# Optimization experiments

Measured on AMD Instinct MI355X. Metric: run time of the kernel, lower is better.

The kernel has to match this reference:

```python
import jax, jax.numpy as jnp
import numpy as np

G = 4096              # number of graphs in batch
NPG = 198             # nodes per graph (fixed by view(-1, 198*2))
N = G * NPG           # total nodes = 811008
DEG = 8               # avg degree
E = N * DEG           # total edges = 6488064
CONV_DIMS = [(2, 20), (20, 15), (15, 10), (10, 5), (5, 2)]
MLP_DIMS = [(396, 200), (200, 100), (100, 50), (50, 10), (10, 2)]


def setup_inputs() -> dict:
    key = jax.random.key(0)
    ks = jax.random.split(key, 64)
    x = jax.random.normal(ks[0], (N, 2), dtype=jnp.float32)
    # block-diagonal edges: endpoints within each 198-node graph, then offset
    src = jax.random.randint(ks[1], (G, E // G), 0, NPG)
    dst = jax.random.randint(ks[2], (G, E // G), 0, NPG)
    off = (jnp.arange(G, dtype=jnp.int32) * NPG)[:, None]
    edge_index = jnp.stack([(src + off).reshape(-1), (dst + off).reshape(-1)]).astype(jnp.int32)
    edge_weight = jax.random.uniform(ks[3], (E,), dtype=jnp.float32)
    inp = {"x": x, "edge_index": edge_index, "edge_weight": edge_weight}
    ki = 4
    for i, (ci, co) in enumerate(CONV_DIMS):
        s = 1.0 / np.sqrt(ci)
        inp[f"w_rel{i}"] = jax.random.normal(ks[ki], (co, ci), jnp.float32) * s; ki += 1
        inp[f"b_rel{i}"] = jax.random.normal(ks[ki], (co,), jnp.float32) * s; ki += 1
        inp[f"w_root{i}"] = jax.random.normal(ks[ki], (co, ci), jnp.float32) * s; ki += 1
    for i, (ci, co) in enumerate(MLP_DIMS):
        s = 1.0 / np.sqrt(ci)
        inp[f"lw{i}"] = jax.random.normal(ks[ki], (co, ci), jnp.float32) * s; ki += 1
        inp[f"lb{i}"] = jax.random.normal(ks[ki], (co,), jnp.float32) * s; ki += 1
    return inp


def _graph_conv(x, src, dst, ew, w_rel, b_rel, w_root):
    # PyG GraphConv: lin_rel(sum_{j->i} e_ji * x_j) + lin_root(x_i)
    msg = x[src] * ew[:, None]                               # [E, Cin] gather
    agg = jax.ops.segment_sum(msg, dst, num_segments=N)      # [N, Cin] scatter-add
    return agg @ w_rel.T + b_rel + x @ w_root.T              # [N, Cout]


def reference(x, edge_index, edge_weight,
              w_rel0, b_rel0, w_root0, w_rel1, b_rel1, w_root1,
              w_rel2, b_rel2, w_root2, w_rel3, b_rel3, w_root3,
              w_rel4, b_rel4, w_root4,
              lw0, lb0, lw1, lb1, lw2, lb2, lw3, lb3, lw4, lb4):
    src, dst = edge_index[0], edge_index[1]
    convs = [(w_rel0, b_rel0, w_root0), (w_rel1, b_rel1, w_root1),
             (w_rel2, b_rel2, w_root2), (w_rel3, b_rel3, w_root3),
             (w_rel4, b_rel4, w_root4)]
    h = x
    for wr, br, wroot in convs:
        h = jax.nn.relu(_graph_conv(h, src, dst, edge_weight, wr, br, wroot))
    h = h.reshape(-1, NPG * 2)                               # [G, 396]
    mlp = [(lw0, lb0), (lw1, lb1), (lw2, lb2), (lw3, lb3)]
    for w, b in mlp:
        h = jax.nn.relu(h @ w.T + b)
    logits = h @ lw4.T + lb4                                 # [G, 2]
    return jax.nn.softmax(logits, axis=1)
```

## Files before the change

### kernel.cpp

```cpp
#include <hip/hip_runtime.h>
#include <hip/hip_fp16.h>

#define NG    4096
#define NPG   198
#define EPG   1584
#define ETOT  (NG * EPG)

#define BC2(u) __builtin_bit_cast(__half2, (u))

typedef _Float16 f16x4 __attribute__((ext_vector_type(4)));
typedef float    f32x4 __attribute__((ext_vector_type(4)));

#define H_F16S    (NG * 396)
#define WTB1_OFF  83200
#define WTB2_OFF  106496
#define WTB3_OFF  113664
#define WTB_TOTAL 114688

__global__ __launch_bounds__(256) void wtrans16_kernel(
    const float* __restrict__ w0, const float* __restrict__ w1,
    const float* __restrict__ w2, const float* __restrict__ w3,
    _Float16* __restrict__ wtb)
{
    const int idx = blockIdx.x * 256 + threadIdx.x;
    const float* w; int K, N, NPAD, rel;
    if (idx < 83200)       { w = w0; K = 396; N = 200; NPAD = 208; rel = idx; }
    else if (idx < 106496) { w = w1; K = 200; N = 100; NPAD = 112; rel = idx - 83200; }
    else if (idx < 113664) { w = w2; K = 100; N = 50;  NPAD = 64;  rel = idx - 106496; }
    else                   { w = w3; K = 50;  N = 10;  NPAD = 16;  rel = idx - 113664; }
    const int span = NPAD * 16;
    const int kc = rel / span;
    const int r  = rel - kc * span;
    const int n  = r >> 4, ki = r & 15;
    const int k  = kc * 16 + ki;
    const float v = (n < N && k < K) ? w[n * K + k] : 0.f;
    wtb[idx] = (_Float16)v;
}


template <int CIN, int COUT, int SIN, int SOUT>
__device__ __forceinline__ void conv_layer_h(
    const unsigned* __restrict__ h_in,
    unsigned* __restrict__ h_out,
    const unsigned* __restrict__ s_edge,
    const unsigned* __restrict__ row_start,
    const unsigned* __restrict__ perm,
    const float* __restrict__ wrel, const float* __restrict__ brel,
    const float* __restrict__ wroot, int tid)
{
    if (tid >= NPG) return;
    const int node = (int)perm[tid];
    constexpr int MS = (CIN + 1) / 2;

    __half2 ms[MS];
#pragma unroll
    for (int p = 0; p < MS; ++p) ms[p] = __floats2half2_rn(0.f, 0.f);

    const unsigned jb = row_start[node], je = row_start[node + 1];
    for (unsigned j = jb; j < je; ++j) {
        const unsigned e  = s_edge[j];
        const __half2  w2 = BC2((e >> 16) * 0x10001u);
        const unsigned* row = h_in + (e & 0xFFFFu) * SIN;
        if constexpr (SIN == 1) {
            ms[0] = __hfma2(w2, BC2(row[0]), ms[0]);
        } else {
            const uint4 q0 = *(const uint4*)row;
            ms[0] = __hfma2(w2, BC2(q0.x), ms[0]);
            if constexpr (MS > 1) ms[1] = __hfma2(w2, BC2(q0.y), ms[1]);
            if constexpr (MS > 2) ms[2] = __hfma2(w2, BC2(q0.z), ms[2]);
            if constexpr (MS > 3) ms[3] = __hfma2(w2, BC2(q0.w), ms[3]);
            if constexpr (MS > 4) {
                const uint4 q1 = *(const uint4*)(row + 4);
                ms[4] = __hfma2(w2, BC2(q1.x), ms[4]);
                if constexpr (MS > 5) ms[5] = __hfma2(w2, BC2(q1.y), ms[5]);
                if constexpr (MS > 6) ms[6] = __hfma2(w2, BC2(q1.z), ms[6]);
                if constexpr (MS > 7) ms[7] = __hfma2(w2, BC2(q1.w), ms[7]);
            }
            if constexpr (MS > 8) {
                const uint4 q2 = *(const uint4*)(row + 8);
                ms[8] = __hfma2(w2, BC2(q2.x), ms[8]);
                if constexpr (MS > 9) ms[9] = __hfma2(w2, BC2(q2.y), ms[9]);
            }
        }
    }

    float aggf[CIN];
#pragma unroll
    for (int p = 0; p < MS; ++p) {
        const float2 fa = __half22float2(ms[p]);
        aggf[2 * p] = fa.x;
        if (2 * p + 1 < CIN) aggf[2 * p + 1] = fa.y;
    }

    float hv[CIN];
    {
        const unsigned* me = h_in + node * SIN;
        unsigned mw[MS];
        if constexpr (SIN == 1) {
            mw[0] = me[0];
        } else {
            const uint4 q0 = *(const uint4*)me;
            mw[0] = q0.x;
            if constexpr (MS > 1) mw[1] = q0.y;
            if constexpr (MS > 2) mw[2] = q0.z;
            if constexpr (MS > 3) mw[3] = q0.w;
            if constexpr (MS > 4) {
                const uint4 q1 = *(const uint4*)(me + 4);
                mw[4] = q1.x;
                if constexpr (MS > 5) mw[5] = q1.y;
                if constexpr (MS > 6) mw[6] = q1.z;
                if constexpr (MS > 7) mw[7] = q1.w;
            }
            if constexpr (MS > 8) {
                const uint4 q2 = *(const uint4*)(me + 8);
                mw[8] = q2.x;
                if constexpr (MS > 9) mw[9] = q2.y;
            }
        }
#pragma unroll
        for (int p = 0; p < MS; ++p) {
            const float2 f = __half22float2(BC2(mw[p]));
            hv[2 * p] = f.x;
            if (2 * p + 1 < CIN) hv[2 * p + 1] = f.y;
        }
    }

    float outv[COUT];
#pragma unroll
    for (int o = 0; o < COUT; ++o) {
        float acc = brel[o];
#pragma unroll
        for (int c = 0; c < CIN; ++c) {
            acc = fmaf(aggf[c], wrel[o * CIN + c], acc);
            acc = fmaf(hv[c],   wroot[o * CIN + c], acc);
        }
        outv[o] = fmaxf(acc, 0.f);
    }

    if constexpr (SOUT == 1) {
        h_out[node] = __builtin_bit_cast(unsigned,
            __floats2half2_rn(outv[0], COUT > 1 ? outv[1] : 0.f));
    } else {
        constexpr int W  = (COUT + 1) / 2;
        constexpr int WQ = (W + 3) / 4;
        unsigned ow[WQ * 4];
#pragma unroll
        for (int p = 0; p < WQ * 4; ++p) {
            const float lo = (2 * p     < COUT) ? outv[2 * p]     : 0.f;
            const float hi = (2 * p + 1 < COUT) ? outv[2 * p + 1] : 0.f;
            ow[p] = __builtin_bit_cast(unsigned, __floats2half2_rn(lo, hi));
        }
        unsigned* orow = h_out + node * SOUT;
#pragma unroll
        for (int q = 0; q < WQ; ++q)
            *(uint4*)(orow + 4 * q) =
                make_uint4(ow[4*q], ow[4*q+1], ow[4*q+2], ow[4*q+3]);
    }
}

__global__ __launch_bounds__(256) void conv_kernel(
    const float* __restrict__ x,
    const int*   __restrict__ eidx,
    const float* __restrict__ ew,
    const float* wr0, const float* br0, const float* wq0,
    const float* wr1, const float* br1, const float* wq1,
    const float* wr2, const float* br2, const float* wq2,
    const float* wr3, const float* br3, const float* wq3,
    const float* wr4, const float* br4, const float* wq4,
    _Float16* __restrict__ H)
{
    __shared__ __align__(16) unsigned s_edge[EPG];
    __shared__ unsigned cnt[256];
    __shared__ unsigned cursor[256];
    __shared__ unsigned row_start[NPG + 1];
    __shared__ unsigned wsum[4];
    __shared__ unsigned dhist[64];
    __shared__ unsigned dcur[64];
    __shared__ unsigned perm[NPG];
    __shared__ __align__(16) unsigned bufA[NPG * 12];
    __shared__ __align__(16) unsigned bufB[NPG * 12];

    const int g = blockIdx.x, tid = threadIdx.x;
    const int ebase = g * EPG, nbase = g * NPG;
    const int lane = tid & 63, wid = tid >> 6;

    const int4*   s4 = (const int4*)(eidx + ebase);
    const int4*   d4 = (const int4*)(eidx + ETOT + ebase);
    const float4* w4 = (const float4*)(ew + ebase);
    const int4   sa = s4[tid];
    const int4   da = d4[tid];
    const float4 wa = w4[tid];
    const bool hasb = tid < (EPG / 4 - 256);
    int4 sb = {0,0,0,0}, db = {0,0,0,0}; float4 wb = {0,0,0,0};
    if (hasb) { sb = s4[tid + 256]; db = d4[tid + 256]; wb = w4[tid + 256]; }

    cnt[tid] = 0u;
    __syncthreads();
    atomicAdd(&cnt[da.x - nbase], 1u); atomicAdd(&cnt[da.y - nbase], 1u);
    atomicAdd(&cnt[da.z - nbase], 1u); atomicAdd(&cnt[da.w - nbase], 1u);
    if (hasb) {
        atomicAdd(&cnt[db.x - nbase], 1u); atomicAdd(&cnt[db.y - nbase], 1u);
        atomicAdd(&cnt[db.z - nbase], 1u); atomicAdd(&cnt[db.w - nbase], 1u);
    }
    __syncthreads();

    const unsigned v = cnt[tid];
    unsigned inc = v;
#pragma unroll
    for (int s = 1; s < 64; s <<= 1) {
        const unsigned t = (unsigned)__shfl_up((int)inc, s);
        if (lane >= s) inc += t;
    }
    if (lane == 63) wsum[wid] = inc;
    __syncthreads();
    unsigned pre = 0;
    for (int w = 0; w < wid; ++w) pre += wsum[w];
    const unsigned excl = pre + inc - v;
    if (tid <= NPG) row_start[tid] = excl;
    if (tid < NPG)  cursor[tid]    = excl;
    __syncthreads();

    {
        auto place = [&](int s, int d, float w) {
            const int dl = d - nbase;
            const unsigned slot = atomicAdd(&cursor[dl], 1u);
            const __half hw = __float2half_rn(w);
            s_edge[slot] = ((unsigned)__half_as_ushort(hw) << 16)
                         | (unsigned)(s - nbase);
        };
        place(sa.x, da.x, wa.x); place(sa.y, da.y, wa.y);
        place(sa.z, da.z, wa.z); place(sa.w, da.w, wa.w);
        if (hasb) {
            place(sb.x, db.x, wb.x); place(sb.y, db.y, wb.y);
            place(sb.z, db.z, wb.z); place(sb.w, db.w, wb.w);
        }
    }

    if (tid < NPG) {
        const float2 xv = ((const float2*)x)[nbase + tid];
        bufA[tid] = __builtin_bit_cast(unsigned, __floats2half2_rn(xv.x, xv.y));
    }

    if (tid < 64) dhist[tid] = 0u;
    __syncthreads();
    unsigned mydeg = 0u;
    if (tid < NPG) {
        mydeg = cnt[tid]; if (mydeg > 63u) mydeg = 63u;
        atomicAdd(&dhist[mydeg], 1u);
    }
    __syncthreads();
    if (tid < 64) {
        const unsigned dv = dhist[tid];
        unsigned sc = dv;
#pragma unroll
        for (int s = 1; s < 64; s <<= 1) {
            const unsigned t = (unsigned)__shfl_up((int)sc, s);
            if (lane >= s) sc += t;
        }
        dcur[tid] = sc - dv;
    }
    __syncthreads();
    if (tid < NPG) {
        const unsigned pos = atomicAdd(&dcur[mydeg], 1u);
        perm[pos] = (unsigned)tid;
    }
    __syncthreads();

    conv_layer_h<2,  20, 1,  12>(bufA, bufB, s_edge, row_start, perm, wr0, br0, wq0, tid);
    __syncthreads();
    conv_layer_h<20, 15, 12, 12>(bufB, bufA, s_edge, row_start, perm, wr1, br1, wq1, tid);
    __syncthreads();
    conv_layer_h<15, 10, 12, 12>(bufA, bufB, s_edge, row_start, perm, wr2, br2, wq2, tid);
    __syncthreads();
    conv_layer_h<10, 5,  12, 12>(bufB, bufA, s_edge, row_start, perm, wr3, br3, wq3, tid);
    __syncthreads();
    conv_layer_h<5,  2,  12, 1 >(bufA, bufB, s_edge, row_start, perm, wr4, br4, wq4, tid);
    __syncthreads();

    if (tid < NPG)
        ((unsigned*)H)[g * 198 + tid] = bufB[tid];
}


__device__ __forceinline__ void zero_words(void* p, int nwords, int tid)
{
    unsigned* u = (unsigned*)p;
    for (int i = tid; i < nwords; i += 256) u[i] = 0u;
}

template<int KC, int NTT, int NOUT, int SIN, int SOUT>
__device__ __forceinline__ void mfma_layer(
    const _Float16* __restrict__ inb,
    _Float16* __restrict__ outb,
    const _Float16* __restrict__ wtb,
    const float* __restrict__ bias, int tid)
{
    constexpr int NPAD = NTT * 16;
    const int lane = tid & 63, wid = tid >> 6;
    const int lrow = lane & 15, lgrp = lane >> 4;
    const _Float16* aptr = inb + lrow * SIN + lgrp * 4;

    for (int nt0 = wid; nt0 < NTT; nt0 += 8) {
        const int  nt1  = nt0 + 4;
        const bool has2 = nt1 < NTT;
        f32x4 acc0 = {0.f, 0.f, 0.f, 0.f};
        f32x4 acc1 = {0.f, 0.f, 0.f, 0.f};
        const int n0 = nt0 * 16 + lrow;
        const int n1 = nt1 * 16 + lrow;
        const _Float16* b0 = wtb + n0 * 16 + lgrp * 4;
        const _Float16* b1 = wtb + n1 * 16 + lgrp * 4;
#pragma unroll 4
        for (int kc = 0; kc < KC; ++kc) {
            const f16x4 a   = *(const f16x4*)(aptr + kc * 16);
            const f16x4 vb0 = *(const f16x4*)(b0 + (size_t)kc * (NPAD * 16));
            acc0 = __builtin_amdgcn_mfma_f32_16x16x16f16(a, vb0, acc0, 0, 0, 0);
            if (has2) {
                const f16x4 vb1 = *(const f16x4*)(b1 + (size_t)kc * (NPAD * 16));
                acc1 = __builtin_amdgcn_mfma_f32_16x16x16f16(a, vb1, acc1, 0, 0, 0);
            }
        }
        if (n0 < NOUT) {
            const float bv = bias[n0];
#pragma unroll
            for (int j = 0; j < 4; ++j)
                outb[(lgrp * 4 + j) * SOUT + n0] =
                    (_Float16)fmaxf(acc0[j] + bv, 0.f);
        }
        if (has2 && n1 < NOUT) {
            const float bv = bias[n1];
#pragma unroll
            for (int j = 0; j < 4; ++j)
                outb[(lgrp * 4 + j) * SOUT + n1] =
                    (_Float16)fmaxf(acc1[j] + bv, 0.f);
        }
    }
}

__global__ __launch_bounds__(256) void mlp_mfma_kernel(
    const _Float16* __restrict__ H,
    const _Float16* __restrict__ wtb,
    const float* __restrict__ lb0, const float* __restrict__ lb1,
    const float* __restrict__ lb2, const float* __restrict__ lb3,
    const float* __restrict__ lw4, const float* __restrict__ lb4,
    float* __restrict__ out)
{
    __shared__ __align__(16) _Float16 bufH[16 * 400];
    __shared__ __align__(16) _Float16 bufX[16 * 224];
    __shared__ __align__(16) _Float16 bufY[16 * 128];

    const int tid   = threadIdx.x;
    const int gbase = blockIdx.x * 16;

    {
        const unsigned* Hw = (const unsigned*)H + (size_t)gbase * 198;
        unsigned* bH = (unsigned*)bufH;
        for (int t = tid; t < 16 * 200; t += 256) {
            const int gg = t / 200, w = t - gg * 200;
            bH[gg * 200 + w] = (w < 198) ? Hw[gg * 198 + w] : 0u;
        }
        zero_words(bufX, 16 * 224 / 2, tid);
        zero_words(bufY, 16 * 128 / 2, tid);
    }
    __syncthreads();

    mfma_layer<25, 13, 200, 400, 224>(bufH, bufX, wtb, lb0, tid);
    __syncthreads();

    zero_words(bufH, 512, tid);
    mfma_layer<13, 7, 100, 224, 128>(bufX, bufY, wtb + WTB1_OFF, lb1, tid);
    __syncthreads();

    zero_words(bufX, 128, tid);
    mfma_layer<7, 4, 50, 128, 64>(bufY, bufH, wtb + WTB2_OFF, lb2, tid);
    __syncthreads();

    mfma_layer<4, 1, 10, 64, 16>(bufH, bufX, wtb + WTB3_OFF, lb3, tid);
    __syncthreads();

    if (tid < 16) {
        float l0 = lb4[0], l1 = lb4[1];
#pragma unroll
        for (int k = 0; k < 10; ++k) {
            const float hv = (float)bufX[tid * 16 + k];
            l0 = fmaf(hv, lw4[k],      l0);
            l1 = fmaf(hv, lw4[10 + k], l1);
        }
        const float m  = fmaxf(l0, l1);
        const float e0 = __expf(l0 - m), e1 = __expf(l1 - m);
        const float inv = 1.f / (e0 + e1);
        float2 p; p.x = e0 * inv; p.y = e1 * inv;
        ((float2*)out)[gbase + tid] = p;
    }
}

extern "C" void kernel_launch(void* const* d_in, const int* in_sizes, int n_in,
                              void* d_out, int out_size, void* d_ws, size_t ws_size,
                              hipStream_t stream)
{
    const float* x    = (const float*)d_in[0];
    const int*   eidx = (const int*)  d_in[1];
    const float* ew   = (const float*)d_in[2];

    const float* wr[5]; const float* br[5]; const float* wq[5];
    for (int i = 0; i < 5; ++i) {
        wr[i] = (const float*)d_in[3 + 3 * i];
        br[i] = (const float*)d_in[4 + 3 * i];
        wq[i] = (const float*)d_in[5 + 3 * i];
    }
    const float* lw[5]; const float* lb[5];
    for (int i = 0; i < 5; ++i) {
        lw[i] = (const float*)d_in[18 + 2 * i];
        lb[i] = (const float*)d_in[19 + 2 * i];
    }

    _Float16* wsH = (_Float16*)d_ws;
    _Float16* wtb = wsH + (size_t)H_F16S;

    wtrans16_kernel<<<(WTB_TOTAL + 255) / 256, 256, 0, stream>>>(
        lw[0], lw[1], lw[2], lw[3], wtb);

    conv_kernel<<<NG, 256, 0, stream>>>(
        x, eidx, ew,
        wr[0], br[0], wq[0],
        wr[1], br[1], wq[1],
        wr[2], br[2], wq[2],
        wr[3], br[3], wq[3],
        wr[4], br[4], wq[4],
        wsH);

    mlp_mfma_kernel<<<NG / 16, 256, 0, stream>>>(
        wsH, wtb,
        lb[0], lb[1], lb[2], lb[3],
        lw[4], lb[4],
        (float*)d_out);
}
```

Baseline: 129.6 us.

## Split graph conv into gather plus MFMA dense transform with fp16 weight staging

Each conv layer is split into a per-node gather stage, which accumulates the edge-weighted neighbour features in fp32 into a shared aggregate buffer, and a dense stage that applies the rel and root linear maps with 16x16x16 fp16 MFMA instructions over node tiles. A new pre-kernel converts the conv weights into padded fp16 MFMA tile layouts. Edge storage changes from packed half weight plus index to separate ushort source and float weight arrays, and the node feature buffers get a wider padded stride. This replaces per-thread scalar FMA loops over weights read from global memory, but it adds an extra __syncthreads per layer, a third shared buffer that raises LDS use and may lower occupancy, buffer zeroing, and an extra kernel launch.

```diff
diff --git a/kernel.cpp b/kernel.cpp
--- a/kernel.cpp
+++ b/kernel.cpp
@@ -5,6 +5,7 @@
 #define NPG   198
 #define EPG   1584
 #define ETOT  (NG * EPG)
+#define SH    24
 
 #define BC2(u) __builtin_bit_cast(__half2, (u))
 
@@ -16,6 +17,7 @@
 #define WTB2_OFF  106496
 #define WTB3_OFF  113664
 #define WTB_TOTAL 114688
+#define CB_TOTAL  3584
 
 __global__ __launch_bounds__(256) void wtrans16_kernel(
     const float* __restrict__ w0, const float* __restrict__ w1,
@@ -23,6 +25,7 @@
     _Float16* __restrict__ wtb)
 {
     const int idx = blockIdx.x * 256 + threadIdx.x;
+    if (idx >= WTB_TOTAL) return;
     const float* w; int K, N, NPAD, rel;
     if (idx < 83200)       { w = w0; K = 396; N = 200; NPAD = 208; rel = idx; }
     else if (idx < 106496) { w = w1; K = 200; N = 100; NPAD = 112; rel = idx - 83200; }
@@ -37,124 +40,117 @@
     wtb[idx] = (_Float16)v;
 }
 
-
-template <int CIN, int COUT, int SIN, int SOUT>
-__device__ __forceinline__ void conv_layer_h(
-    const unsigned* __restrict__ h_in,
-    unsigned* __restrict__ h_out,
-    const unsigned* __restrict__ s_edge,
-    const unsigned* __restrict__ row_start,
-    const unsigned* __restrict__ perm,
-    const float* __restrict__ wrel, const float* __restrict__ brel,
-    const float* __restrict__ wroot, int tid)
+__global__ __launch_bounds__(256) void wconv16_kernel(
+    const float* wr0, const float* wq0, const float* wr1, const float* wq1,
+    const float* wr2, const float* wq2, const float* wr3, const float* wq3,
+    const float* wr4, const float* wq4, _Float16* __restrict__ cb)
+{
+    const int idx = blockIdx.x * 256 + threadIdx.x;
+    if (idx >= CB_TOTAL) return;
+    const float* w; int CIN, COUT, NT, q;
+    if (idx < 1024)      { CIN = 2;  COUT = 20; NT = 2; int r = idx;        int h = r >= 512; q = r - h * 512; w = h ? wq0 : wr0; }
+    else if (idx < 2048) { CIN = 20; COUT = 15; NT = 1; int r = idx - 1024; int h = r >= 512; q = r - h * 512; w = h ? wq1 : wr1; }
+    else if (idx < 2560) { CIN = 15; COUT = 10; NT = 1; int r = idx - 2048; int h = r >= 256; q = r - h * 256; w = h ? wq2 : wr2; }
+    else if (idx < 3072) { CIN = 10; COUT = 5;  NT = 1; int r = idx - 2560; int h = r >= 256; q = r - h * 256; w = h ? wq3 : wr3; }
+    else                 { CIN = 5;  COUT = 2;  NT = 1; int r = idx - 3072; int h = r >= 256; q = r - h * 256; w = h ? wq4 : wr4; }
+    const int chunk = NT * 256;
+    const int kc = q / chunk, r2 = q - kc * chunk;
+    const int n = r2 >> 4, ki = r2 & 15, k = kc * 16 + ki;
+    const float v = (n < COUT && k < CIN) ? w[n * CIN + k] : 0.f;
+    cb[idx] = (_Float16)v;
+}
+
+template <int CIN>
+__device__ __forceinline__ void conv_gather(
+    const _Float16* __restrict__ bufIn, _Float16* __restrict__ bufAgg,
+    const unsigned short* __restrict__ s_src, const float* __restrict__ s_ewf,
+    const unsigned* __restrict__ row_start, const unsigned* __restrict__ perm,
+    int tid)
 {
     if (tid >= NPG) return;
     const int node = (int)perm[tid];
     constexpr int MS = (CIN + 1) / 2;
-
-    __half2 ms[MS];
-#pragma unroll
-    for (int p = 0; p < MS; ++p) ms[p] = __floats2half2_rn(0.f, 0.f);
+    constexpr int NW = ((MS + 3) / 4) * 4;
+
+    float acc[CIN];
+#pragma unroll
+    for (int c = 0; c < CIN; ++c) acc[c] = 0.f;
 
     const unsigned jb = row_start[node], je = row_start[node + 1];
     for (unsigned j = jb; j < je; ++j) {
-        const unsigned e  = s_edge[j];
-        const __half2  w2 = BC2((e >> 16) * 0x10001u);
-        const unsigned* row = h_in + (e & 0xFFFFu) * SIN;
-        if constexpr (SIN == 1) {
-            ms[0] = __hfma2(w2, BC2(row[0]), ms[0]);
+        const int   src = (int)s_src[j];
+        const float w   = s_ewf[j];
+        const unsigned* rw = (const unsigned*)(bufIn + src * SH);
+        unsigned wv[NW];
+        if constexpr (MS == 1) {
+            wv[0] = rw[0];
         } else {
-            const uint4 q0 = *(const uint4*)row;
-            ms[0] = __hfma2(w2, BC2(q0.x), ms[0]);
-            if constexpr (MS > 1) ms[1] = __hfma2(w2, BC2(q0.y), ms[1]);
-            if constexpr (MS > 2) ms[2] = __hfma2(w2, BC2(q0.z), ms[2]);
-            if constexpr (MS > 3) ms[3] = __hfma2(w2, BC2(q0.w), ms[3]);
-            if constexpr (MS > 4) {
-                const uint4 q1 = *(const uint4*)(row + 4);
-                ms[4] = __hfma2(w2, BC2(q1.x), ms[4]);
-                if constexpr (MS > 5) ms[5] = __hfma2(w2, BC2(q1.y), ms[5]);
-                if constexpr (MS > 6) ms[6] = __hfma2(w2, BC2(q1.z), ms[6]);
-                if constexpr (MS > 7) ms[7] = __hfma2(w2, BC2(q1.w), ms[7]);
+#pragma unroll
+            for (int qn = 0; qn < NW / 4; ++qn) {
+                const uint4 q = ((const uint4*)rw)[qn];
+                wv[4*qn] = q.x; wv[4*qn+1] = q.y; wv[4*qn+2] = q.z; wv[4*qn+3] = q.w;
             }
-            if constexpr (MS > 8) {
-                const uint4 q2 = *(const uint4*)(row + 8);
-                ms[8] = __hfma2(w2, BC2(q2.x), ms[8]);
-                if constexpr (MS > 9) ms[9] = __hfma2(w2, BC2(q2.y), ms[9]);
+        }
+#pragma unroll
+        for (int p = 0; p < MS; ++p) {
+            const float2 f = __half22float2(BC2(wv[p]));
+            acc[2*p] = fmaf(w, f.x, acc[2*p]);
+            if (2*p + 1 < CIN) acc[2*p+1] = fmaf(w, f.y, acc[2*p+1]);
+        }
+    }
+
+    unsigned ow[12];
+#pragma unroll
+    for (int p = 0; p < 12; ++p) {
+        const float lo = (2*p     < CIN) ? acc[2*p]     : 0.f;
+        const float hi = (2*p + 1 < CIN) ? acc[2*p + 1] : 0.f;
+        ow[p] = __builtin_bit_cast(unsigned, __floats2half2_rn(lo, hi));
+    }
+    unsigned* orow = (unsigned*)(bufAgg + node * SH);
+#pragma unroll
+    for (int qn = 0; qn < 3; ++qn)
+        ((uint4*)orow)[qn] = make_uint4(ow[4*qn], ow[4*qn+1], ow[4*qn+2], ow[4*qn+3]);
+}
+
+template <int CIN, int COUT, int KCA, int NT>
+__device__ __forceinline__ void conv_dense(
+    const _Float16* __restrict__ bufIn,
+    const _Float16* __restrict__ bufAgg,
+    _Float16* __restrict__ bufOut,
+    const _Float16* __restrict__ wbrel, const _Float16* __restrict__ wbroot,
+    const float* __restrict__ bias, int tid)
+{
+    const int lane = tid & 63, wid = tid >> 6;
+    const int lrow = lane & 15, lgrp = lane >> 4;
+
+    for (int p = wid; p < 13 * NT; p += 4) {
+        const int mt = p / NT, nt = p - mt * NT;
+        const int arow = mt * 16 + lrow;
+        const _Float16* aA = bufAgg + arow * SH + lgrp * 4;
+        const _Float16* aH = bufIn  + arow * SH + lgrp * 4;
+        const int n = nt * 16 + lrow;
+        const _Float16* bR = wbrel  + n * 16 + lgrp * 4;
+        const _Float16* bT = wbroot + n * 16 + lgrp * 4;
+
+        f32x4 acc = {0.f, 0.f, 0.f, 0.f};
+#pragma unroll
+        for (int kc = 0; kc < KCA; ++kc) {
+            acc = __builtin_amdgcn_mfma_f32_16x16x16f16(
+                *(const f16x4*)(aA + kc * 16),
+                *(const f16x4*)(bR + kc * (NT * 256)), acc, 0, 0, 0);
+            acc = __builtin_amdgcn_mfma_f32_16x16x16f16(
+                *(const f16x4*)(aH + kc * 16),
+                *(const f16x4*)(bT + kc * (NT * 256)), acc, 0, 0, 0);
+        }
+        if (n < COUT) {
+            const float bv = bias[n];
+#pragma unroll
+            for (int j = 0; j < 4; ++j) {
+                const int r = mt * 16 + lgrp * 4 + j;
+                if (r < NPG)
+                    bufOut[r * SH + n] = (_Float16)fmaxf(acc[j] + bv, 0.f);
             }
         }
-    }
-
-    float aggf[CIN];
-#pragma unroll
-    for (int p = 0; p < MS; ++p) {
-        const float2 fa = __half22float2(ms[p]);
-        aggf[2 * p] = fa.x;
-        if (2 * p + 1 < CIN) aggf[2 * p + 1] = fa.y;
-    }
-
-    float hv[CIN];
-    {
-        const unsigned* me = h_in + node * SIN;
-        unsigned mw[MS];
-        if constexpr (SIN == 1) {
-            mw[0] = me[0];
-        } else {
-            const uint4 q0 = *(const uint4*)me;
-            mw[0] = q0.x;
-            if constexpr (MS > 1) mw[1] = q0.y;
-            if constexpr (MS > 2) mw[2] = q0.z;
-            if constexpr (MS > 3) mw[3] = q0.w;
-            if constexpr (MS > 4) {
-                const uint4 q1 = *(const uint4*)(me + 4);
-                mw[4] = q1.x;
-                if constexpr (MS > 5) mw[5] = q1.y;
-                if constexpr (MS > 6) mw[6] = q1.z;
-                if constexpr (MS > 7) mw[7] = q1.w;
-            }
-            if constexpr (MS > 8) {
-                const uint4 q2 = *(const uint4*)(me + 8);
-                mw[8] = q2.x;
-                if constexpr (MS > 9) mw[9] = q2.y;
-            }
-        }
-#pragma unroll
-        for (int p = 0; p < MS; ++p) {
-            const float2 f = __half22float2(BC2(mw[p]));
-            hv[2 * p] = f.x;
-            if (2 * p + 1 < CIN) hv[2 * p + 1] = f.y;
-        }
-    }
-
-    float outv[COUT];
-#pragma unroll
-    for (int o = 0; o < COUT; ++o) {
-        float acc = brel[o];
-#pragma unroll
-        for (int c = 0; c < CIN; ++c) {
-            acc = fmaf(aggf[c], wrel[o * CIN + c], acc);
-            acc = fmaf(hv[c],   wroot[o * CIN + c], acc);
-        }
-        outv[o] = fmaxf(acc, 0.f);
-    }
-
-    if constexpr (SOUT == 1) {
-        h_out[node] = __builtin_bit_cast(unsigned,
-            __floats2half2_rn(outv[0], COUT > 1 ? outv[1] : 0.f));
-    } else {
-        constexpr int W  = (COUT + 1) / 2;
-        constexpr int WQ = (W + 3) / 4;
-        unsigned ow[WQ * 4];
-#pragma unroll
-        for (int p = 0; p < WQ * 4; ++p) {
-            const float lo = (2 * p     < COUT) ? outv[2 * p]     : 0.f;
-            const float hi = (2 * p + 1 < COUT) ? outv[2 * p + 1] : 0.f;
-            ow[p] = __builtin_bit_cast(unsigned, __floats2half2_rn(lo, hi));
-        }
-        unsigned* orow = h_out + node * SOUT;
-#pragma unroll
-        for (int q = 0; q < WQ; ++q)
-            *(uint4*)(orow + 4 * q) =
-                make_uint4(ow[4*q], ow[4*q+1], ow[4*q+2], ow[4*q+3]);
     }
 }
 
@@ -162,14 +158,14 @@
     const float* __restrict__ x,
     const int*   __restrict__ eidx,
     const float* __restrict__ ew,
-    const float* wr0, const float* br0, const float* wq0,
-    const float* wr1, const float* br1, const float* wq1,
-    const float* wr2, const float* br2, const float* wq2,
-    const float* wr3, const float* br3, const float* wq3,
-    const float* wr4, const float* br4, const float* wq4,
+    const float* __restrict__ br0, const float* __restrict__ br1,
+    const float* __restrict__ br2, const float* __restrict__ br3,
+    const float* __restrict__ br4,
+    const _Float16* __restrict__ cb,
     _Float16* __restrict__ H)
 {
-    __shared__ __align__(16) unsigned s_edge[EPG];
+    __shared__ unsigned short s_src[EPG];
+    __shared__ float          s_ewf[EPG];
     __shared__ unsigned cnt[256];
     __shared__ unsigned cursor[256];
     __shared__ unsigned row_start[NPG + 1];
@@ -177,12 +173,22 @@
     __shared__ unsigned dhist[64];
     __shared__ unsigned dcur[64];
     __shared__ unsigned perm[NPG];
-    __shared__ __align__(16) unsigned bufA[NPG * 12];
-    __shared__ __align__(16) unsigned bufB[NPG * 12];
+    __shared__ __align__(16) _Float16 bufA[208 * SH + 32];
+    __shared__ __align__(16) _Float16 bufB[208 * SH + 32];
+    __shared__ __align__(16) _Float16 bufG[208 * SH + 32];
 
     const int g = blockIdx.x, tid = threadIdx.x;
     const int ebase = g * EPG, nbase = g * NPG;
     const int lane = tid & 63, wid = tid >> 6;
+
+    {
+        unsigned* zA = (unsigned*)bufA;
+        unsigned* zB = (unsigned*)bufB;
+        unsigned* zG = (unsigned*)bufG;
+        for (int i = tid; i < (208 * SH + 32) / 2; i += 256) {
+            zA[i] = 0u; zB[i] = 0u; zG[i] = 0u;
+        }
+    }
 
     const int4*   s4 = (const int4*)(eidx + ebase);
     const int4*   d4 = (const int4*)(eidx + ETOT + ebase);
@@ -224,9 +230,8 @@
         auto place = [&](int s, int d, float w) {
             const int dl = d - nbase;
             const unsigned slot = atomicAdd(&cursor[dl], 1u);
-            const __half hw = __float2half_rn(w);
-            s_edge[slot] = ((unsigned)__half_as_ushort(hw) << 16)
-                         | (unsigned)(s - nbase);
+            s_src[slot] = (unsigned short)(s - nbase);
+            s_ewf[slot] = w;
         };
         place(sa.x, da.x, wa.x); place(sa.y, da.y, wa.y);
         place(sa.z, da.z, wa.z); place(sa.w, da.w, wa.w);
@@ -238,7 +243,8 @@
 
     if (tid < NPG) {
         const float2 xv = ((const float2*)x)[nbase + tid];
-        bufA[tid] = __builtin_bit_cast(unsigned, __floats2half2_rn(xv.x, xv.y));
+        *(unsigned*)(bufA + tid * SH) =
+            __builtin_bit_cast(unsigned, __floats2half2_rn(xv.x, xv.y));
     }
 
     if (tid < 64) dhist[tid] = 0u;
@@ -266,21 +272,23 @@
     }
     __syncthreads();
 
-    conv_layer_h<2,  20, 1,  12>(bufA, bufB, s_edge, row_start, perm, wr0, br0, wq0, tid);
-    __syncthreads();
-    conv_layer_h<20, 15, 12, 12>(bufB, bufA, s_edge, row_start, perm, wr1, br1, wq1, tid);
-    __syncthreads();
-    conv_layer_h<15, 10, 12, 12>(bufA, bufB, s_edge, row_start, perm, wr2, br2, wq2, tid);
-    __syncthreads();
-    conv_layer_h<10, 5,  12, 12>(bufB, bufA, s_edge, row_start, perm, wr3, br3, wq3, tid);
-    __syncthreads();
-    conv_layer_h<5,  2,  12, 1 >(bufA, bufB, s_edge, row_start, perm, wr4, br4, wq4, tid);
-    __syncthreads();
+#define LAYER(CIN, COUT, KCA, NT, FIN, FOUT, RELOFF, ROOTOFF, BR)             \
+    conv_gather<CIN>(FIN, bufG, s_src, s_ewf, row_start, perm, tid);          \
+    __syncthreads();                                                          \
+    conv_dense<CIN, COUT, KCA, NT>(FIN, bufG, FOUT, cb + RELOFF,              \
+                                   cb + ROOTOFF, BR, tid);                    \
+    __syncthreads();
+
+    LAYER(2,  20, 1, 2, bufA, bufB, 0,    512,  br0)
+    LAYER(20, 15, 2, 1, bufB, bufA, 1024, 1536, br1)
+    LAYER(15, 10, 1, 1, bufA, bufB, 2048, 2304, br2)
+    LAYER(10, 5,  1, 1, bufB, bufA, 2560, 2816, br3)
+    LAYER(5,  2,  1, 1, bufA, bufB, 3072, 3328, br4)
+#undef LAYER
 
     if (tid < NPG)
-        ((unsigned*)H)[g * 198 + tid] = bufB[tid];
-}
-
+        ((unsigned*)H)[g * 198 + tid] = *(const unsigned*)(bufB + tid * SH);
+}
 
 __device__ __forceinline__ void zero_words(void* p, int nwords, int tid)
 {
@@ -415,18 +423,19 @@
 
     _Float16* wsH = (_Float16*)d_ws;
     _Float16* wtb = wsH + (size_t)H_F16S;
+    _Float16* cb  = wtb + (size_t)WTB_TOTAL;
 
     wtrans16_kernel<<<(WTB_TOTAL + 255) / 256, 256, 0, stream>>>(
         lw[0], lw[1], lw[2], lw[3], wtb);
 
+    wconv16_kernel<<<(CB_TOTAL + 255) / 256, 256, 0, stream>>>(
+        wr[0], wq[0], wr[1], wq[1], wr[2], wq[2], wr[3], wq[3], wr[4], wq[4],
+        cb);
+
     conv_kernel<<<NG, 256, 0, stream>>>(
         x, eidx, ew,
-        wr[0], br[0], wq[0],
-        wr[1], br[1], wq[1],
-        wr[2], br[2], wq[2],
-        wr[3], br[3], wq[3],
-        wr[4], br[4], wq[4],
-        wsH);
+        br[0], br[1], br[2], br[3], br[4],
+        cb, wsH);
 
     mlp_mfma_kernel<<<NG / 16, 256, 0, stream>>>(
         wsH, wtb,
```

After: 179.6 us. 1.39x slower.

## Move middle GraphConv dense transforms to MFMA and widen MLP blocks to 512

Applied to the files above, without the earlier changes.

Conv layers 1-3 are split into two steps. A gather step writes the aggregated neighbour features to a shared buffer, and an MFMA 16x16x16 f16 step then applies the rel and root weights, which a new kernel pre-packs into f16 tiles. Edge aggregation now accumulates in fp32 instead of half2, and row_start and perm become 16-bit arrays. The MLP kernel moves to 512 threads with one N-tile per wave. This adds extra syncs, a third shared buffer (more LDS, which may lower occupancy) and zero-initialisation of all three buffers.

```diff
diff --git a/kernel.cpp b/kernel.cpp
--- a/kernel.cpp
+++ b/kernel.cpp
@@ -5,6 +5,8 @@
 #define NPG   198
 #define EPG   1584
 #define ETOT  (NG * EPG)
+#define SHW   12
+#define NROW  208
 
 #define BC2(u) __builtin_bit_cast(__half2, (u))
 
@@ -16,6 +18,7 @@
 #define WTB2_OFF  106496
 #define WTB3_OFF  113664
 #define WTB_TOTAL 114688
+#define CB_TOTAL  3584
 
 __global__ __launch_bounds__(256) void wtrans16_kernel(
     const float* __restrict__ w0, const float* __restrict__ w1,
@@ -23,6 +26,7 @@
     _Float16* __restrict__ wtb)
 {
     const int idx = blockIdx.x * 256 + threadIdx.x;
+    if (idx >= WTB_TOTAL) return;
     const float* w; int K, N, NPAD, rel;
     if (idx < 83200)       { w = w0; K = 396; N = 200; NPAD = 208; rel = idx; }
     else if (idx < 106496) { w = w1; K = 200; N = 100; NPAD = 112; rel = idx - 83200; }
@@ -37,14 +41,33 @@
     wtb[idx] = (_Float16)v;
 }
 
+__global__ __launch_bounds__(256) void wconv16_kernel(
+    const float* wr0, const float* wq0, const float* wr1, const float* wq1,
+    const float* wr2, const float* wq2, const float* wr3, const float* wq3,
+    const float* wr4, const float* wq4, _Float16* __restrict__ cb)
+{
+    const int idx = blockIdx.x * 256 + threadIdx.x;
+    if (idx >= CB_TOTAL) return;
+    const float* w; int CIN, COUT, NT, q;
+    if (idx < 1024)      { CIN = 2;  COUT = 20; NT = 2; int r = idx;        int h = r >= 512; q = r - h * 512; w = h ? wq0 : wr0; }
+    else if (idx < 2048) { CIN = 20; COUT = 15; NT = 1; int r = idx - 1024; int h = r >= 512; q = r - h * 512; w = h ? wq1 : wr1; }
+    else if (idx < 2560) { CIN = 15; COUT = 10; NT = 1; int r = idx - 2048; int h = r >= 256; q = r - h * 256; w = h ? wq2 : wr2; }
+    else if (idx < 3072) { CIN = 10; COUT = 5;  NT = 1; int r = idx - 2560; int h = r >= 256; q = r - h * 256; w = h ? wq3 : wr3; }
+    else                 { CIN = 5;  COUT = 2;  NT = 1; int r = idx - 3072; int h = r >= 256; q = r - h * 256; w = h ? wq4 : wr4; }
+    const int chunk = NT * 256;
+    const int kc = q / chunk, r2 = q - kc * chunk;
+    const int n = r2 >> 4, ki = r2 & 15, k = kc * 16 + ki;
+    const float v = (n < COUT && k < CIN) ? w[n * CIN + k] : 0.f;
+    cb[idx] = (_Float16)v;
+}
 
 template <int CIN, int COUT, int SIN, int SOUT>
 __device__ __forceinline__ void conv_layer_h(
     const unsigned* __restrict__ h_in,
     unsigned* __restrict__ h_out,
     const unsigned* __restrict__ s_edge,
-    const unsigned* __restrict__ row_start,
-    const unsigned* __restrict__ perm,
+    const unsigned short* __restrict__ row_start,
+    const unsigned short* __restrict__ perm,
     const float* __restrict__ wrel, const float* __restrict__ brel,
     const float* __restrict__ wroot, int tid)
 {
@@ -52,76 +75,53 @@
     const int node = (int)perm[tid];
     constexpr int MS = (CIN + 1) / 2;
 
-    __half2 ms[MS];
-#pragma unroll
-    for (int p = 0; p < MS; ++p) ms[p] = __floats2half2_rn(0.f, 0.f);
+    float aggf[MS * 2];
+#pragma unroll
+    for (int c = 0; c < MS * 2; ++c) aggf[c] = 0.f;
 
     const unsigned jb = row_start[node], je = row_start[node + 1];
     for (unsigned j = jb; j < je; ++j) {
         const unsigned e  = s_edge[j];
-        const __half2  w2 = BC2((e >> 16) * 0x10001u);
+        const float    wf = __half2float(__ushort_as_half((unsigned short)(e >> 16)));
         const unsigned* row = h_in + (e & 0xFFFFu) * SIN;
+        unsigned wv[MS];
         if constexpr (SIN == 1) {
-            ms[0] = __hfma2(w2, BC2(row[0]), ms[0]);
+            wv[0] = row[0];
         } else {
             const uint4 q0 = *(const uint4*)row;
-            ms[0] = __hfma2(w2, BC2(q0.x), ms[0]);
-            if constexpr (MS > 1) ms[1] = __hfma2(w2, BC2(q0.y), ms[1]);
-            if constexpr (MS > 2) ms[2] = __hfma2(w2, BC2(q0.z), ms[2]);
-            if constexpr (MS > 3) ms[3] = __hfma2(w2, BC2(q0.w), ms[3]);
+            wv[0] = q0.x;
+            if constexpr (MS > 1) wv[1] = q0.y;
+            if constexpr (MS > 2) wv[2] = q0.z;
+            if constexpr (MS > 3) wv[3] = q0.w;
             if constexpr (MS > 4) {
                 const uint4 q1 = *(const uint4*)(row + 4);
-                ms[4] = __hfma2(w2, BC2(q1.x), ms[4]);
-                if constexpr (MS > 5) ms[5] = __hfma2(w2, BC2(q1.y), ms[5]);
-                if constexpr (MS > 6) ms[6] = __hfma2(w2, BC2(q1.z), ms[6]);
-                if constexpr (MS > 7) ms[7] = __hfma2(w2, BC2(q1.w), ms[7]);
+                wv[4] = q1.x;
+                if constexpr (MS > 5) wv[5] = q1.y;
+                if constexpr (MS > 6) wv[6] = q1.z;
+                if constexpr (MS > 7) wv[7] = q1.w;
             }
             if constexpr (MS > 8) {
                 const uint4 q2 = *(const uint4*)(row + 8);
-                ms[8] = __hfma2(w2, BC2(q2.x), ms[8]);
-                if constexpr (MS > 9) ms[9] = __hfma2(w2, BC2(q2.y), ms[9]);
+                wv[8] = q2.x;
+                if constexpr (MS > 9) wv[9] = q2.y;
             }
         }
-    }
-
-    float aggf[CIN];
-#pragma unroll
-    for (int p = 0; p < MS; ++p) {
-        const float2 fa = __half22float2(ms[p]);
-        aggf[2 * p] = fa.x;
-        if (2 * p + 1 < CIN) aggf[2 * p + 1] = fa.y;
-    }
-
-    float hv[CIN];
+#pragma unroll
+        for (int p = 0; p < MS; ++p) {
+            const __half2 h2 = BC2(wv[p]);
+            aggf[2*p]     = fmaf(wf, __low2float(h2),  aggf[2*p]);
+            aggf[2*p + 1] = fmaf(wf, __high2float(h2), aggf[2*p + 1]);
+        }
+    }
+
+    float hv[MS * 2];
     {
         const unsigned* me = h_in + node * SIN;
-        unsigned mw[MS];
-        if constexpr (SIN == 1) {
-            mw[0] = me[0];
-        } else {
-            const uint4 q0 = *(const uint4*)me;
-            mw[0] = q0.x;
-            if constexpr (MS > 1) mw[1] = q0.y;
-            if constexpr (MS > 2) mw[2] = q0.z;
-            if constexpr (MS > 3) mw[3] = q0.w;
-            if constexpr (MS > 4) {
-                const uint4 q1 = *(const uint4*)(me + 4);
-                mw[4] = q1.x;
-                if constexpr (MS > 5) mw[5] = q1.y;
-                if constexpr (MS > 6) mw[6] = q1.z;
-                if constexpr (MS > 7) mw[7] = q1.w;
-            }
-            if constexpr (MS > 8) {
-                const uint4 q2 = *(const uint4*)(me + 8);
-                mw[8] = q2.x;
-                if constexpr (MS > 9) mw[9] = q2.y;
-            }
-        }
 #pragma unroll
         for (int p = 0; p < MS; ++p) {
-            const float2 f = __half22float2(BC2(mw[p]));
-            hv[2 * p] = f.x;
-            if (2 * p + 1 < CIN) hv[2 * p + 1] = f.y;
+            const __half2 h2 = BC2(me[p]);
+            hv[2*p]     = __low2float(h2);
+            hv[2*p + 1] = __high2float(h2);
         }
     }
 
@@ -141,20 +141,117 @@
         h_out[node] = __builtin_bit_cast(unsigned,
             __floats2half2_rn(outv[0], COUT > 1 ? outv[1] : 0.f));
     } else {
-        constexpr int W  = (COUT + 1) / 2;
-        constexpr int WQ = (W + 3) / 4;
-        unsigned ow[WQ * 4];
-#pragma unroll
-        for (int p = 0; p < WQ * 4; ++p) {
+        unsigned ow[SOUT];
+#pragma unroll
+        for (int p = 0; p < SOUT; ++p) {
             const float lo = (2 * p     < COUT) ? outv[2 * p]     : 0.f;
             const float hi = (2 * p + 1 < COUT) ? outv[2 * p + 1] : 0.f;
             ow[p] = __builtin_bit_cast(unsigned, __floats2half2_rn(lo, hi));
         }
         unsigned* orow = h_out + node * SOUT;
 #pragma unroll
-        for (int q = 0; q < WQ; ++q)
-            *(uint4*)(orow + 4 * q) =
-                make_uint4(ow[4*q], ow[4*q+1], ow[4*q+2], ow[4*q+3]);
+        for (int qn = 0; qn < SOUT / 4; ++qn)
+            *(uint4*)(orow + 4 * qn) =
+                make_uint4(ow[4*qn], ow[4*qn+1], ow[4*qn+2], ow[4*qn+3]);
+    }
+}
+
+template <int CIN>
+__device__ __forceinline__ void gather_to_G(
+    const unsigned* __restrict__ fin, unsigned* __restrict__ bufG,
+    const unsigned* __restrict__ s_edge,
+    const unsigned short* __restrict__ row_start,
+    const unsigned short* __restrict__ perm, int tid)
+{
+    if (tid >= NPG) return;
+    const int node = (int)perm[tid];
+    constexpr int MS = (CIN + 1) / 2;
+
+    float acc[MS * 2];
+#pragma unroll
+    for (int c = 0; c < MS * 2; ++c) acc[c] = 0.f;
+
+    const unsigned jb = row_start[node], je = row_start[node + 1];
+    for (unsigned j = jb; j < je; ++j) {
+        const unsigned e  = s_edge[j];
+        const float    wf = __half2float(__ushort_as_half((unsigned short)(e >> 16)));
+        const unsigned* row = fin + (e & 0xFFFFu) * SHW;
+        unsigned wv[MS];
+        const uint4 q0 = *(const uint4*)row;
+        wv[0] = q0.x;
+        if constexpr (MS > 1) wv[1] = q0.y;
+        if constexpr (MS > 2) wv[2] = q0.z;
+        if constexpr (MS > 3) wv[3] = q0.w;
+        if constexpr (MS > 4) {
+            const uint4 q1 = *(const uint4*)(row + 4);
+            wv[4] = q1.x;
+            if constexpr (MS > 5) wv[5] = q1.y;
+            if constexpr (MS > 6) wv[6] = q1.z;
+            if constexpr (MS > 7) wv[7] = q1.w;
+        }
+        if constexpr (MS > 8) {
+            const uint4 q2 = *(const uint4*)(row + 8);
+            wv[8] = q2.x;
+            if constexpr (MS > 9) wv[9] = q2.y;
+        }
+#pragma unroll
+        for (int p = 0; p < MS; ++p) {
+            const __half2 h2 = BC2(wv[p]);
+            acc[2*p]     = fmaf(wf, __low2float(h2),  acc[2*p]);
+            acc[2*p + 1] = fmaf(wf, __high2float(h2), acc[2*p + 1]);
+        }
+    }
+
+    unsigned ow[SHW];
+#pragma unroll
+    for (int p = 0; p < SHW; ++p)
+        ow[p] = (p < MS)
+            ? __builtin_bit_cast(unsigned, __floats2half2_rn(acc[2*p], acc[2*p+1]))
+            : 0u;
+    unsigned* orow = bufG + node * SHW;
+#pragma unroll
+    for (int qn = 0; qn < SHW / 4; ++qn)
+        *(uint4*)(orow + 4 * qn) =
+            make_uint4(ow[4*qn], ow[4*qn+1], ow[4*qn+2], ow[4*qn+3]);
+}
+
+template <int CIN, int COUT, int KCA>
+__device__ __forceinline__ void conv_dense(
+    const _Float16* __restrict__ bufRoot,
+    const _Float16* __restrict__ bufAgg,
+    _Float16* __restrict__ bufOut,
+    const _Float16* __restrict__ wbrel, const _Float16* __restrict__ wbroot,
+    const float* __restrict__ bias, int tid)
+{
+    const int lane = tid & 63, wid = tid >> 6;
+    const int lrow = lane & 15, lgrp = lane >> 4;
+
+    for (int mt = wid; mt < 13; mt += 4) {
+        const int arow = mt * 16 + lrow;
+        const _Float16* aA = bufAgg  + arow * 24 + lgrp * 4;
+        const _Float16* aH = bufRoot + arow * 24 + lgrp * 4;
+        const _Float16* bR = wbrel  + lrow * 16 + lgrp * 4;
+        const _Float16* bT = wbroot + lrow * 16 + lgrp * 4;
+
+        f32x4 acc = {0.f, 0.f, 0.f, 0.f};
+#pragma unroll
+        for (int kc = 0; kc < KCA; ++kc) {
+            acc = __builtin_amdgcn_mfma_f32_16x16x16f16(
+                *(const f16x4*)(aA + kc * 16),
+                *(const f16x4*)(bR + kc * 256), acc, 0, 0, 0);
+            acc = __builtin_amdgcn_mfma_f32_16x16x16f16(
+                *(const f16x4*)(aH + kc * 16),
+                *(const f16x4*)(bT + kc * 256), acc, 0, 0, 0);
+        }
+        if (lrow < COUT) {
+            const float bv = bias[lrow];
+#pragma unroll
+            for (int j = 0; j < 4; ++j) {
+                const int r = mt * 16 + lgrp * 4 + j;
+                if (r < NPG)
+                    bufOut[r * 24 + lrow] = (_Float16)fmaxf(acc[j] + bv, 0.f);
+            }
+        }
     }
 }
 
@@ -162,27 +259,34 @@
     const float* __restrict__ x,
     const int*   __restrict__ eidx,
     const float* __restrict__ ew,
-    const float* wr0, const float* br0, const float* wq0,
-    const float* wr1, const float* br1, const float* wq1,
-    const float* wr2, const float* br2, const float* wq2,
-    const float* wr3, const float* br3, const float* wq3,
-    const float* wr4, const float* br4, const float* wq4,
+    const float* __restrict__ wr0, const float* __restrict__ br0,
+    const float* __restrict__ wq0,
+    const float* __restrict__ br1, const float* __restrict__ br2,
+    const float* __restrict__ br3,
+    const float* __restrict__ wr4, const float* __restrict__ br4,
+    const float* __restrict__ wq4,
+    const _Float16* __restrict__ cb,
     _Float16* __restrict__ H)
 {
     __shared__ __align__(16) unsigned s_edge[EPG];
-    __shared__ unsigned cnt[256];
-    __shared__ unsigned cursor[256];
-    __shared__ unsigned row_start[NPG + 1];
-    __shared__ unsigned wsum[4];
-    __shared__ unsigned dhist[64];
-    __shared__ unsigned dcur[64];
-    __shared__ unsigned perm[NPG];
-    __shared__ __align__(16) unsigned bufA[NPG * 12];
-    __shared__ __align__(16) unsigned bufB[NPG * 12];
+    __shared__ unsigned       cnt[256];
+    __shared__ unsigned       cursor[256];
+    __shared__ unsigned short row_start[NPG + 2];
+    __shared__ unsigned       wsum[4];
+    __shared__ unsigned       dhist[64];
+    __shared__ unsigned       dcur[64];
+    __shared__ unsigned short perm[NPG + 2];
+    __shared__ __align__(16) unsigned bufA[NROW * SHW];
+    __shared__ __align__(16) unsigned bufB[NROW * SHW];
+    __shared__ __align__(16) unsigned bufG[NROW * SHW];
 
     const int g = blockIdx.x, tid = threadIdx.x;
     const int ebase = g * EPG, nbase = g * NPG;
     const int lane = tid & 63, wid = tid >> 6;
+
+    for (int i = tid; i < NROW * SHW; i += 256) {
+        bufA[i] = 0u; bufB[i] = 0u; bufG[i] = 0u;
+    }
 
     const int4*   s4 = (const int4*)(eidx + ebase);
     const int4*   d4 = (const int4*)(eidx + ETOT + ebase);
@@ -216,7 +320,7 @@
     unsigned pre = 0;
     for (int w = 0; w < wid; ++w) pre += wsum[w];
     const unsigned excl = pre + inc - v;
-    if (tid <= NPG) row_start[tid] = excl;
+    if (tid <= NPG) row_start[tid] = (unsigned short)excl;
     if (tid < NPG)  cursor[tid]    = excl;
     __syncthreads();
 
@@ -245,7 +349,7 @@
     __syncthreads();
     unsigned mydeg = 0u;
     if (tid < NPG) {
-        mydeg = cnt[tid]; if (mydeg > 63u) mydeg = 63u;
+        mydeg = v; if (mydeg > 63u) mydeg = 63u;
         atomicAdd(&dhist[mydeg], 1u);
     }
     __syncthreads();
@@ -262,30 +366,48 @@
     __syncthreads();
     if (tid < NPG) {
         const unsigned pos = atomicAdd(&dcur[mydeg], 1u);
-        perm[pos] = (unsigned)tid;
-    }
-    __syncthreads();
-
-    conv_layer_h<2,  20, 1,  12>(bufA, bufB, s_edge, row_start, perm, wr0, br0, wq0, tid);
-    __syncthreads();
-    conv_layer_h<20, 15, 12, 12>(bufB, bufA, s_edge, row_start, perm, wr1, br1, wq1, tid);
-    __syncthreads();
-    conv_layer_h<15, 10, 12, 12>(bufA, bufB, s_edge, row_start, perm, wr2, br2, wq2, tid);
-    __syncthreads();
-    conv_layer_h<10, 5,  12, 12>(bufB, bufA, s_edge, row_start, perm, wr3, br3, wq3, tid);
-    __syncthreads();
-    conv_layer_h<5,  2,  12, 1 >(bufA, bufB, s_edge, row_start, perm, wr4, br4, wq4, tid);
+        perm[pos] = (unsigned short)tid;
+    }
+    __syncthreads();
+
+    const _Float16* fA = (const _Float16*)bufA;
+    const _Float16* fB = (const _Float16*)bufB;
+    const _Float16* fG = (const _Float16*)bufG;
+
+    conv_layer_h<2, 20, 1, SHW>(bufA, bufB, s_edge, row_start, perm,
+                                wr0, br0, wq0, tid);
+    __syncthreads();
+
+    gather_to_G<20>(bufB, bufG, s_edge, row_start, perm, tid);
+    __syncthreads();
+    conv_dense<20, 15, 2>(fB, fG, (_Float16*)bufA, cb + 1024, cb + 1536,
+                          br1, tid);
+    __syncthreads();
+
+    gather_to_G<15>(bufA, bufG, s_edge, row_start, perm, tid);
+    __syncthreads();
+    conv_dense<15, 10, 1>(fA, fG, (_Float16*)bufB, cb + 2048, cb + 2304,
+                          br2, tid);
+    __syncthreads();
+
+    gather_to_G<10>(bufB, bufG, s_edge, row_start, perm, tid);
+    __syncthreads();
+    conv_dense<10, 5, 1>(fB, fG, (_Float16*)bufA, cb + 2560, cb + 2816,
+                         br3, tid);
+    __syncthreads();
+
+    conv_layer_h<5, 2, SHW, 1>(bufA, bufB, s_edge, row_start, perm,
+                               wr4, br4, wq4, tid);
     __syncthreads();
 
     if (tid < NPG)
         ((unsigned*)H)[g * 198 + tid] = bufB[tid];
 }
 
-
 __device__ __forceinline__ void zero_words(void* p, int nwords, int tid)
 {
     unsigned* u = (unsigned*)p;
-    for (int i = tid; i < nwords; i += 256) u[i] = 0u;
+    for (int i = tid; i < nwords; i += 512) u[i] = 0u;
 }
 
 template<int KC, int NTT, int NOUT, int SIN, int SOUT>
@@ -298,45 +420,41 @@
     constexpr int NPAD = NTT * 16;
     const int lane = tid & 63, wid = tid >> 6;
     const int lrow = lane & 15, lgrp = lane >> 4;
+    const int nt0 = wid;
+    if (nt0 >= NTT) return;
+    const bool has2 = (nt0 + 8) < NTT;
     const _Float16* aptr = inb + lrow * SIN + lgrp * 4;
 
-    for (int nt0 = wid; nt0 < NTT; nt0 += 8) {
-        const int  nt1  = nt0 + 4;
-        const bool has2 = nt1 < NTT;
-        f32x4 acc0 = {0.f, 0.f, 0.f, 0.f};
-        f32x4 acc1 = {0.f, 0.f, 0.f, 0.f};
-        const int n0 = nt0 * 16 + lrow;
-        const int n1 = nt1 * 16 + lrow;
-        const _Float16* b0 = wtb + n0 * 16 + lgrp * 4;
-        const _Float16* b1 = wtb + n1 * 16 + lgrp * 4;
+    f32x4 acc0 = {0.f, 0.f, 0.f, 0.f};
+    f32x4 acc1 = {0.f, 0.f, 0.f, 0.f};
+    const int n0 = nt0 * 16 + lrow;
+    const int n1 = (nt0 + 8) * 16 + lrow;
+    const _Float16* b0 = wtb + n0 * 16 + lgrp * 4;
+    const _Float16* b1 = wtb + n1 * 16 + lgrp * 4;
 #pragma unroll 4
-        for (int kc = 0; kc < KC; ++kc) {
-            const f16x4 a   = *(const f16x4*)(aptr + kc * 16);
-            const f16x4 vb0 = *(const f16x4*)(b0 + (size_t)kc * (NPAD * 16));
-            acc0 = __builtin_amdgcn_mfma_f32_16x16x16f16(a, vb0, acc0, 0, 0, 0);
-            if (has2) {
-                const f16x4 vb1 = *(const f16x4*)(b1 + (size_t)kc * (NPAD * 16));
-                acc1 = __builtin_amdgcn_mfma_f32_16x16x16f16(a, vb1, acc1, 0, 0, 0);
-            }
-        }
-        if (n0 < NOUT) {
-            const float bv = bias[n0];
-#pragma unroll
-            for (int j = 0; j < 4; ++j)
-                outb[(lgrp * 4 + j) * SOUT + n0] =
-                    (_Float16)fmaxf(acc0[j] + bv, 0.f);
-        }
-        if (has2 && n1 < NOUT) {
-            const float bv = bias[n1];
-#pragma unroll
-            for (int j = 0; j < 4; ++j)
-                outb[(lgrp * 4 + j) * SOUT + n1] =
-                    (_Float16)fmaxf(acc1[j] + bv, 0.f);
-        }
-    }
-}
-
-__global__ __launch_bounds__(256) void mlp_mfma_kernel(
+    for (int kc = 0; kc < KC; ++kc) {
+        const f16x4 a = *(const f16x4*)(aptr + kc * 16);
+        acc0 = __builtin_amdgcn_mfma_f32_16x16x16f16(
+            a, *(const f16x4*)(b0 + (size_t)kc * (NPAD * 16)), acc0, 0, 0, 0);
+        if (has2)
+            acc1 = __builtin_amdgcn_mfma_f32_16x16x16f16(
+                a, *(const f16x4*)(b1 + (size_t)kc * (NPAD * 16)), acc1, 0, 0, 0);
+    }
+    if (n0 < NOUT) {
+        const float bv = bias[n0];
+#pragma unroll
+        for (int j = 0; j < 4; ++j)
+            outb[(lgrp * 4 + j) * SOUT + n0] = (_Float16)fmaxf(acc0[j] + bv, 0.f);
+    }
+    if (has2 && n1 < NOUT) {
+        const float bv = bias[n1];
+#pragma unroll
+        for (int j = 0; j < 4; ++j)
+            outb[(lgrp * 4 + j) * SOUT + n1] = (_Float16)fmaxf(acc1[j] + bv, 0.f);
+    }
+}
+
+__global__ __launch_bounds__(512) void mlp_mfma_kernel(
     const _Float16* __restrict__ H,
     const _Float16* __restrict__ wtb,
     const float* __restrict__ lb0, const float* __restrict__ lb1,
@@ -354,7 +472,7 @@
     {
         const unsigned* Hw = (const unsigned*)H + (size_t)gbase * 198;
         unsigned* bH = (unsigned*)bufH;
-        for (int t = tid; t < 16 * 200; t += 256) {
+        for (int t = tid; t < 16 * 200; t += 512) {
             const int gg = t / 200, w = t - gg * 200;
             bH[gg * 200 + w] = (w < 198) ? Hw[gg * 198 + w] : 0u;
         }
@@ -415,20 +533,23 @@
 
     _Float16* wsH = (_Float16*)d_ws;
     _Float16* wtb = wsH + (size_t)H_F16S;
+    _Float16* cb  = wtb + (size_t)WTB_TOTAL;
 
     wtrans16_kernel<<<(WTB_TOTAL + 255) / 256, 256, 0, stream>>>(
         lw[0], lw[1], lw[2], lw[3], wtb);
+
+    wconv16_kernel<<<(CB_TOTAL + 255) / 256, 256, 0, stream>>>(
+        wr[0], wq[0], wr[1], wq[1], wr[2], wq[2], wr[3], wq[3], wr[4], wq[4],
+        cb);
 
     conv_kernel<<<NG, 256, 0, stream>>>(
         x, eidx, ew,
         wr[0], br[0], wq[0],
-        wr[1], br[1], wq[1],
-        wr[2], br[2], wq[2],
-        wr[3], br[3], wq[3],
+        br[1], br[2], br[3],
         wr[4], br[4], wq[4],
-        wsH);
-
-    mlp_mfma_kernel<<<NG / 16, 256, 0, stream>>>(
+        cb, wsH);
+
+    mlp_mfma_kernel<<<NG / 16, 512, 0, stream>>>(
         wsH, wtb,
         lb[0], lb[1], lb[2], lb[3],
         lw[4], lb[4],
```

Result: faster. 123.3 us (-4.8%).
